# Performance work log

Measured on AMD Instinct MI355X. Metric: run time of the kernel, lower is better.

The kernel has to match this reference:

```python
import jax, jax.numpy as jnp
import numpy as np

N, M, D = 16384, 4096, 512
TEMP = 1.0


def setup_inputs() -> dict:
    key = jax.random.key(0)
    kx, ky = jax.random.split(key)
    x = jax.random.normal(kx, (N, D), dtype=jnp.float32)
    y = jax.random.normal(ky, (M, D), dtype=jnp.float32)
    return {"x": x, "y": y, "temperature": 1}


def reference(x, y, temperature):
    # euclidean_distances_logits:
    #   logits = -0.5 * T * sum_d (x[n,None,:] - y[None,m,:])**2
    # Fused form avoiding the O(n*m*d) broadcast intermediate (same math):
    t = jnp.asarray(temperature, dtype=x.dtype) * jnp.float32(TEMP)
    x_sq = jnp.sum(x * x, axis=1, keepdims=True)          # [n, 1]
    y_sq = jnp.sum(y * y, axis=1)[None, :]                # [1, m]
    xy = jnp.einsum("nd,md->nm", x, y)                    # [n, m]
    sq_dist = x_sq - 2.0 * xy + y_sq                      # [n, m]
    return -0.5 * t * sq_dist
```

## Files before the change

### kernel.cpp

```cpp
#include <hip/hip_runtime.h>
#include <hip/hip_bf16.h>


#define NN 16384
#define MM 4096
#define DD 512

using frag_ab = __attribute__((ext_vector_type(8))) short;
using floatx4 = __attribute__((ext_vector_type(4))) float;

using gas_ptr = const __attribute__((address_space(1))) void*;
using las_ptr = __attribute__((address_space(3))) void*;

__device__ __forceinline__ void async_copy16(const void* g, void* l) {
    __builtin_amdgcn_global_load_lds((gas_ptr)g, (las_ptr)l, 16, 0, 0);
}

__device__ __forceinline__ unsigned bf16rne(float f) {
    union { float f; unsigned u; } v; v.f = f;
    unsigned u = v.u + 0x7FFFu + ((v.u >> 16) & 1u);
    return u >> 16;
}

__device__ __forceinline__ uint2 cvt4(float4 v) {
    uint2 r;
    r.x = bf16rne(v.x) | (bf16rne(v.y) << 16);
    r.y = bf16rne(v.z) | (bf16rne(v.w) << 16);
    return r;
}

__global__ void prep_all(const float* __restrict__ x, const float* __restrict__ y,
                         float* __restrict__ xsq, float* __restrict__ ysq,
                         unsigned short* __restrict__ xb, unsigned short* __restrict__ yb) {
    const int lane = threadIdx.x & 63;
    const int row  = blockIdx.x * 4 + (threadIdx.x >> 6);
    const float* src;
    unsigned short* db;
    float* ds;
    if (row < NN) {
        src = x + (size_t)row * DD; db = xb + (size_t)row * DD; ds = xsq + row;
    } else {
        const int r = row - NN;
        src = y + (size_t)r * DD; db = yb + (size_t)r * DD; ds = ysq + r;
    }
    const float* p = src + lane * 8;
    float4 a = *(const float4*)(p);
    float4 b = *(const float4*)(p + 4);
    uint2 lo = cvt4(a), hi = cvt4(b);
    *(uint4*)(db + lane * 8) = make_uint4(lo.x, lo.y, hi.x, hi.y);
    float s = a.x*a.x + a.y*a.y + a.z*a.z + a.w*a.w
            + b.x*b.x + b.y*b.y + b.z*b.z + b.w*b.w;
    #pragma unroll
    for (int off = 32; off > 0; off >>= 1) s += __shfl_xor(s, off);
    if (lane == 0) *ds = s;
}

__global__ void rowsq_kernel(const float* __restrict__ v, float* __restrict__ sq) {
    const int lane = threadIdx.x & 63;
    const int row  = blockIdx.x * 4 + (threadIdx.x >> 6);
    const float* p = v + (size_t)row * DD + lane * 8;
    float4 a = *(const float4*)(p);
    float4 b = *(const float4*)(p + 4);
    float s = a.x*a.x + a.y*a.y + a.z*a.z + a.w*a.w
            + b.x*b.x + b.y*b.y + b.z*b.z + b.w*b.w;
    #pragma unroll
    for (int off = 32; off > 0; off >>= 1) s += __shfl_xor(s, off);
    if (lane == 0) sq[row] = s;
}

__global__ __launch_bounds__(512, 2) void protonet_gemm_256(
    const unsigned short* __restrict__ xb, const unsigned short* __restrict__ yb,
    const float* __restrict__ xsq, const float* __restrict__ ysq,
    const int* __restrict__ temp, float* __restrict__ out)
{
    __shared__ __align__(16) unsigned short S[65536];

    const int bn   = blockIdx.x;
    const int bm   = blockIdx.y;
    const int tid  = threadIdx.x;
    const int lane = tid & 63;
    const int wave = tid >> 6;
    const int wx   = wave >> 2;
    const int wy   = wave & 3;
    const int l15  = lane & 15;
    const int quad = lane >> 4;

    floatx4 acc[8][4] = {};

    const unsigned short* gsrc[8];
    int loff[8];
    #pragma unroll
    for (int c = 0; c < 8; ++c) {
        const int s  = wave * 8 + c;
        const int ss = s & 31;
        const int rg = ss >> 1;
        const int kh = ss & 1;
        const bool a_side = (s < 32);
        const unsigned short* base = a_side
            ? xb + ((size_t)(bn * 256 + rg * 16 + l15) * DD + kh * 32 + quad * 8)
            : yb + ((size_t)(bm * 256 + rg * 16 + l15) * DD + kh * 32 + quad * 8);
        gsrc[c] = base;
        loff[c] = (a_side ? 0 : 32768) + ss * 512;
    }

    #pragma unroll
    for (int c = 0; c < 8; ++c)
        async_copy16(gsrc[c], S + loff[c]);
    #pragma unroll
    for (int c = 0; c < 8; ++c)
        async_copy16(gsrc[c] + 64, S + loff[c] + 16384);

    #pragma unroll
    for (int t = 0; t < 8; ++t) {
        if (t < 7) asm volatile("s_waitcnt vmcnt(8)" ::: "memory");
        else       asm volatile("s_waitcnt vmcnt(0)" ::: "memory");
        __builtin_amdgcn_s_barrier();
        __builtin_amdgcn_sched_barrier(0);

        const int koff = (t & 1) * 16384;

        frag_ab b[4][2];
        #pragma unroll
        for (int fc = 0; fc < 4; ++fc)
            #pragma unroll
            for (int kh = 0; kh < 2; ++kh)
                b[fc][kh] = *(const frag_ab*)(S + 32768 + koff
                                              + ((wy * 4 + fc) * 2 + kh) * 512 + lane * 8);

        #pragma unroll
        for (int pr = 0; pr < 4; ++pr) {
            frag_ab a[2][2];
            #pragma unroll
            for (int i = 0; i < 2; ++i)
                #pragma unroll
                for (int kh = 0; kh < 2; ++kh)
                    a[i][kh] = *(const frag_ab*)(S + koff
                                  + ((wx * 8 + pr * 2 + i) * 2 + kh) * 512 + lane * 8);
            #pragma unroll
            for (int i = 0; i < 2; ++i)
                #pragma unroll
                for (int fc = 0; fc < 4; ++fc)
                    #pragma unroll
                    for (int kh = 0; kh < 2; ++kh)
                        acc[pr * 2 + i][fc] = __builtin_amdgcn_mfma_f32_16x16x32_bf16(
                            a[i][kh], b[fc][kh], acc[pr * 2 + i][fc], 0, 0, 0);
        }

        __builtin_amdgcn_sched_barrier(0);
        __builtin_amdgcn_s_barrier();
        if (t < 6) {
            const int k0n = (t + 2) * 64;
            const int pko = (t & 1) * 16384;
            #pragma unroll
            for (int c = 0; c < 8; ++c)
                async_copy16(gsrc[c] + k0n, S + loff[c] + pko);
        }
    }

    const float tt = (float)(*temp);
    const int n_base = bn * 256 + wx * 128;
    const int m_base = bm * 256 + wy * 64;
    #pragma unroll
    for (int fr = 0; fr < 8; ++fr) {
        float xs[4];
        #pragma unroll
        for (int r = 0; r < 4; ++r) xs[r] = xsq[n_base + fr * 16 + quad * 4 + r];
        #pragma unroll
        for (int fc = 0; fc < 4; ++fc) {
            const int mcol = m_base + fc * 16 + l15;
            const float ys = ysq[mcol];
            #pragma unroll
            for (int r = 0; r < 4; ++r) {
                const int nrow = n_base + fr * 16 + quad * 4 + r;
                out[(size_t)nrow * MM + mcol] = tt * (acc[fr][fc][r] - 0.5f * (xs[r] + ys));
            }
        }
    }
}

__global__ __launch_bounds__(256) void protonet_gemm(
    const float* __restrict__ x, const float* __restrict__ y,
    const float* __restrict__ xsq, const float* __restrict__ ysq,
    const int* __restrict__ temp, float* __restrict__ out)
{
    __shared__ __align__(16) unsigned short As[128 * 32];
    __shared__ __align__(16) unsigned short Bs[128 * 32];

    const int bn   = blockIdx.x;
    const int bm   = blockIdx.y;
    const int tid  = threadIdx.x;
    const int lane = tid & 63;
    const int wave = tid >> 6;
    const int wn   = wave & 1;
    const int wm   = wave >> 1;
    const int l15  = lane & 15;
    const int quad = lane >> 4;

    floatx4 acc[4][4] = {};

    for (int k0 = 0; k0 < DD; k0 += 32) {
        #pragma unroll
        for (int i = 0; i < 4; ++i) {
            int c = tid + i * 256;
            int row = c >> 3, col4 = c & 7;
            float4 v = *(const float4*)(x + (size_t)(bn * 128 + row) * DD + k0 + col4 * 4);
            *(uint2*)(&As[row * 32 + col4 * 4]) = cvt4(v);
        }
        #pragma unroll
        for (int i = 0; i < 4; ++i) {
            int c = tid + i * 256;
            int row = c >> 3, col4 = c & 7;
            float4 v = *(const float4*)(y + (size_t)(bm * 128 + row) * DD + k0 + col4 * 4);
            *(uint2*)(&Bs[row * 32 + col4 * 4]) = cvt4(v);
        }
        __syncthreads();

        frag_ab a[4], b[4];
        #pragma unroll
        for (int t = 0; t < 4; ++t) {
            a[t] = *(const frag_ab*)(&As[(wn * 64 + t * 16 + l15) * 32 + quad * 8]);
            b[t] = *(const frag_ab*)(&Bs[(wm * 64 + t * 16 + l15) * 32 + quad * 8]);
        }
        #pragma unroll
        for (int tn = 0; tn < 4; ++tn)
            #pragma unroll
            for (int tm = 0; tm < 4; ++tm)
                acc[tn][tm] = __builtin_amdgcn_mfma_f32_16x16x32_bf16(
                    a[tn], b[tm], acc[tn][tm], 0, 0, 0);
        __syncthreads();
    }

    const float t = (float)(*temp);
    const int n_base = bn * 128 + wn * 64;
    const int m_base = bm * 128 + wm * 64;
    #pragma unroll
    for (int tn = 0; tn < 4; ++tn) {
        float xs[4];
        #pragma unroll
        for (int r = 0; r < 4; ++r) xs[r] = xsq[n_base + tn * 16 + quad * 4 + r];
        #pragma unroll
        for (int tm = 0; tm < 4; ++tm) {
            const int mcol = m_base + tm * 16 + l15;
            const float ys = ysq[mcol];
            #pragma unroll
            for (int r = 0; r < 4; ++r) {
                const int nrow = n_base + tn * 16 + quad * 4 + r;
                out[(size_t)nrow * MM + mcol] = t * (acc[tn][tm][r] - 0.5f * (xs[r] + ys));
            }
        }
    }
}

extern "C" void kernel_launch(void* const* d_in, const int* in_sizes, int n_in,
                              void* d_out, int out_size, void* d_ws, size_t ws_size,
                              hipStream_t stream) {
    const float* x    = (const float*)d_in[0];
    const float* y    = (const float*)d_in[1];
    const int*   temp = (const int*)d_in[2];
    float* out = (float*)d_out;

    float* xsq = (float*)d_ws;
    float* ysq = xsq + NN;
    unsigned short* xb = (unsigned short*)(ysq + MM);
    unsigned short* yb = xb + (size_t)NN * DD;

    const size_t need = (size_t)(NN + MM) * 4 + (size_t)(NN + MM) * DD * 2;

    if (ws_size >= need) {
        prep_all<<<(NN + MM) / 4, 256, 0, stream>>>(x, y, xsq, ysq, xb, yb);
        protonet_gemm_256<<<dim3(NN / 256, MM / 256), 512, 0, stream>>>(
            xb, yb, xsq, ysq, temp, out);
    } else {
        rowsq_kernel<<<NN / 4, 256, 0, stream>>>(x, xsq);
        rowsq_kernel<<<MM / 4, 256, 0, stream>>>(y, ysq);
        protonet_gemm<<<dim3(NN / 128, MM / 128), 256, 0, stream>>>(
            x, y, xsq, ysq, temp, out);
    }
}
```

Baseline: 374.1 us.

## Swap MFMA operands for row-contiguous float4 stores and remap blocks per XCD

The MFMA A/B operands are swapped so each lane holds four consecutive output columns. The epilogue can then write float4 vectors instead of scattered scalar stores, and y-norms are loaded as float4. Block indices are also remapped so that consecutive blocks on the same XCD share n-tiles, which is meant to improve L2 reuse of operands. The cost is extra index arithmetic, and the remap assumes a 64x16 grid.

```diff
diff --git a/kernel.cpp b/kernel.cpp
--- a/kernel.cpp
+++ b/kernel.cpp
@@ -75,8 +75,12 @@
 {
     __shared__ __align__(16) unsigned short S[65536];
 
-    const int bn   = blockIdx.x;
-    const int bm   = blockIdx.y;
+    const int lin = blockIdx.x + blockIdx.y * 64;
+    const int xcd = lin & 7;
+    const int idx = lin >> 3;
+    const int bn  = xcd * 8 + (idx & 7);
+    const int bm  = idx >> 3;
+
     const int tid  = threadIdx.x;
     const int lane = tid & 63;
     const int wave = tid >> 6;
@@ -121,11 +125,11 @@
 
         frag_ab b[4][2];
         #pragma unroll
-        for (int fc = 0; fc < 4; ++fc)
+        for (int fb = 0; fb < 4; ++fb)
             #pragma unroll
             for (int kh = 0; kh < 2; ++kh)
-                b[fc][kh] = *(const frag_ab*)(S + 32768 + koff
-                                              + ((wy * 4 + fc) * 2 + kh) * 512 + lane * 8);
+                b[fb][kh] = *(const frag_ab*)(S + 32768 + koff
+                                              + ((wy * 4 + fb) * 2 + kh) * 512 + lane * 8);
 
         #pragma unroll
         for (int pr = 0; pr < 4; ++pr) {
@@ -139,11 +143,11 @@
             #pragma unroll
             for (int i = 0; i < 2; ++i)
                 #pragma unroll
-                for (int fc = 0; fc < 4; ++fc)
+                for (int fb = 0; fb < 4; ++fb)
                     #pragma unroll
                     for (int kh = 0; kh < 2; ++kh)
-                        acc[pr * 2 + i][fc] = __builtin_amdgcn_mfma_f32_16x16x32_bf16(
-                            a[i][kh], b[fc][kh], acc[pr * 2 + i][fc], 0, 0, 0);
+                        acc[pr * 2 + i][fb] = __builtin_amdgcn_mfma_f32_16x16x32_bf16(
+                            b[fb][kh], a[i][kh], acc[pr * 2 + i][fb], 0, 0, 0);
         }
 
         __builtin_amdgcn_sched_barrier(0);
@@ -160,20 +164,26 @@
     const float tt = (float)(*temp);
     const int n_base = bn * 256 + wx * 128;
     const int m_base = bm * 256 + wy * 64;
-    #pragma unroll
-    for (int fr = 0; fr < 8; ++fr) {
-        float xs[4];
-        #pragma unroll
-        for (int r = 0; r < 4; ++r) xs[r] = xsq[n_base + fr * 16 + quad * 4 + r];
-        #pragma unroll
-        for (int fc = 0; fc < 4; ++fc) {
-            const int mcol = m_base + fc * 16 + l15;
-            const float ys = ysq[mcol];
-            #pragma unroll
-            for (int r = 0; r < 4; ++r) {
-                const int nrow = n_base + fr * 16 + quad * 4 + r;
-                out[(size_t)nrow * MM + mcol] = tt * (acc[fr][fc][r] - 0.5f * (xs[r] + ys));
-            }
+
+    float4 ys4[4];
+    #pragma unroll
+    for (int fb = 0; fb < 4; ++fb)
+        ys4[fb] = *(const float4*)(ysq + m_base + fb * 16 + quad * 4);
+
+    #pragma unroll
+    for (int fa = 0; fa < 8; ++fa) {
+        const int nrow = n_base + fa * 16 + l15;
+        const float xs = xsq[nrow];
+        float* orow = out + (size_t)nrow * MM + m_base + quad * 4;
+        #pragma unroll
+        for (int fb = 0; fb < 4; ++fb) {
+            const floatx4 v = acc[fa][fb];
+            float4 o;
+            o.x = tt * (v[0] - 0.5f * (xs + ys4[fb].x));
+            o.y = tt * (v[1] - 0.5f * (xs + ys4[fb].y));
+            o.z = tt * (v[2] - 0.5f * (xs + ys4[fb].z));
+            o.w = tt * (v[3] - 0.5f * (xs + ys4[fb].w));
+            *(float4*)(orow + fb * 16) = o;
         }
     }
 }
```

New measurement: 410.2 us. 9.6% more time.
